# Kernel tuning notes

Measured on AMD Instinct MI355X. Metric: run time of the kernel, lower is better.

## Reference

```python
import jax, jax.numpy as jnp
import numpy as np

B, C, D, E = 2048, 64, 1024, 128
P_INT = 0.0  # p_int=0 -> intervention mask is all zeros (deterministic)


def setup_inputs() -> dict:
    key = jax.random.key(0)
    ks = jax.random.split(key, 16)
    s = lambda k, shape, fan: jax.random.normal(k, shape, jnp.float32) * (1.0 / np.sqrt(fan))
    return {
        "x": jax.random.normal(ks[0], (B, D), jnp.float32),
        "c_int": jax.random.uniform(ks[1], (B, C), jnp.float32),
        # stacked per-concept scorer MLP: Linear(D,D) -> ReLU -> Linear(D,1) -> Sigmoid
        "W1": s(ks[2], (C, D, D), D), "b1": jnp.zeros((C, D), jnp.float32),
        "w2": s(ks[3], (C, D), D), "b2": jnp.zeros((C,), jnp.float32),
        # stacked per-concept embed layer: Linear(D+1, D+1) -> ReLU
        "Wl": s(ks[4], (C, D + 1, D + 1), D + 1), "bl": jnp.zeros((C, D + 1), jnp.float32),
        # shared heads
        "Wmu": s(ks[5], (D + 1, E), D + 1), "bmu": jnp.zeros((E,), jnp.float32),
        "Wlv": s(ks[6], (D + 1, E), D + 1), "blv": jnp.zeros((E,), jnp.float32),
        "proto_pos": jax.random.normal(ks[7], (C, E), jnp.float32),
        "proto_neg": jax.random.normal(ks[8], (C, E), jnp.float32),
    }


def reference(x, c_int, W1, b1, w2, b2, Wl, bl, Wmu, bmu, Wlv, blv, proto_pos, proto_neg):
    # Concept scorers (all concepts batched as one grouped GEMM).
    h = jax.nn.relu(jnp.einsum("bd,cdk->bck", x, W1) + b1)          # [B,C,D]
    c_pred = jax.nn.sigmoid(jnp.einsum("bck,ck->bc", h, w2) + b2)    # [B,C]
    # Per-concept embedding layer on [x ; c_pred].
    xc = jnp.concatenate(
        [jnp.broadcast_to(x[:, None, :], (x.shape[0], C, D)), c_pred[..., None]], axis=-1
    )                                                                # [B,C,D+1]
    emb = jax.nn.relu(jnp.einsum("bck,ckj->bcj", xc, Wl) + bl)       # [B,C,D+1]
    mu = jnp.einsum("bcj,je->bce", emb, Wmu) + bmu                   # [B,C,E]
    logvar = jnp.einsum("bcj,je->bce", emb, Wlv) + blv               # [B,C,E]
    c_emb = mu  # eval mode: no reparameterization noise
    # Intervention blend (mask ~ Bernoulli(p_int); p_int=0 -> zeros, deterministic)
    mask = jnp.zeros_like(c_pred)                                    # [B,C]
    cp = mask * c_int + (1.0 - mask) * c_pred                        # [B,C]
    proto = cp[..., None] * proto_pos + (1.0 - cp[..., None]) * proto_neg  # [B,C,E]
    c_emb = mask[..., None] * proto + (1.0 - mask[..., None]) * c_emb
    return (c_pred, c_emb, mu, logvar)
```

## Files before the change

### kernel.cpp

```cpp
#include <hip/hip_runtime.h>
#include <hip/hip_bf16.h>
#include <cstdint>
#include <cstddef>

#define OFF_CE 131072ull
#define OFF_MU (131072ull + 16777216ull)
#define OFF_LV (131072ull + 33554432ull)

using bf16x8 = __attribute__((ext_vector_type(8))) __bf16;
using s16x8  = __attribute__((ext_vector_type(8))) short;
using f32x4  = __attribute__((ext_vector_type(4))) float;

__device__ __forceinline__ unsigned short f2bf(float x) {
  unsigned u = __builtin_bit_cast(unsigned, x);
  return (unsigned short)((u + 0x7FFFu + ((u >> 16) & 1u)) >> 16);
}
__device__ __forceinline__ float bf2f(unsigned short h) {
  unsigned u = ((unsigned)h) << 16;
  return __builtin_bit_cast(float, u);
}
__device__ __forceinline__ void async16(const void* g, void* l) {
  __builtin_amdgcn_global_load_lds(
      (const __attribute__((address_space(1))) void*)g,
      (__attribute__((address_space(3))) void*)l, 16, 0, 0);
}

struct PX {
  const float *Wl, *Wmu, *Wlv, *b2, *presum, *w2l, *bl1024, *Wlcolf;
  const unsigned short *xb;
  unsigned short *WlT, *WheadT;
  float *whead1024f, *e1024, *pred;
};

template <int ALIGNED, int NT>
__device__ __forceinline__ void tile_tr64(const float* __restrict__ src, int stride,
                                          unsigned short* __restrict__ dst, int t256,
                                          float (*t)[68]) {
#pragma unroll
  for (int i = 0; i < 4; ++i) {
    const int row = (t256 >> 4) + (i << 4);
    const int col4 = (t256 & 15) << 2;
    const float* sp = src + (size_t)row * stride + col4;
    float4 v;
    if constexpr (ALIGNED) {
      v = *(const float4*)sp;
    } else if constexpr (NT) {
      v.x = __builtin_nontemporal_load(sp);
      v.y = __builtin_nontemporal_load(sp + 1);
      v.z = __builtin_nontemporal_load(sp + 2);
      v.w = __builtin_nontemporal_load(sp + 3);
    } else {
      v.x = sp[0]; v.y = sp[1]; v.z = sp[2]; v.w = sp[3];
    }
    *(float4*)&t[row][col4] = v;
  }
  __syncthreads();
  const int n = t256 & 63;
#pragma unroll
  for (int pq = 0; pq < 2; ++pq) {
    const int k8 = ((t256 >> 6) << 3) + (pq << 5);
    unsigned short tmp[8];
#pragma unroll
    for (int j = 0; j < 8; ++j) tmp[j] = f2bf(t[k8 + j][n]);
    *(uint4*)(dst + (size_t)n * 1024 + k8) = *(uint4*)tmp;
  }
}

__global__ __launch_bounds__(256) void prep1_k(const float* __restrict__ W1,
                                               const float* __restrict__ x,
                                               const float* __restrict__ Wl,
                                               const float* __restrict__ bl,
                                               unsigned short* __restrict__ xb,
                                               unsigned short* __restrict__ W1T,
                                               float* __restrict__ wlastf,
                                               float* __restrict__ blpf,
                                               float* __restrict__ Wlcolf,
                                               float* __restrict__ w2l,
                                               float* __restrict__ bl1024) {
  __shared__ float t[64][68];
  const int bid = blockIdx.x;
  const int tid = threadIdx.x;
  if (bid < 16384) {
    const int c = bid >> 8, kt = (bid >> 4) & 15, nt = bid & 15;
    tile_tr64<1, 0>(W1 + ((size_t)c << 20) + ((size_t)(kt << 6) << 10) + (nt << 6), 1024,
                    W1T + ((size_t)c << 20) + ((size_t)(nt << 6) << 10) + (kt << 6), tid, t);
  } else if (bid < 17408) {
    const int idx = (bid - 16384) * 256 + tid;
    const float4* xv = (const float4*)x;
    float4 a = xv[idx * 2], b = xv[idx * 2 + 1];
    unsigned w0 = f2bf(a.x) | ((unsigned)f2bf(a.y) << 16);
    unsigned w1 = f2bf(a.z) | ((unsigned)f2bf(a.w) << 16);
    unsigned w2 = f2bf(b.x) | ((unsigned)f2bf(b.y) << 16);
    unsigned w3 = f2bf(b.z) | ((unsigned)f2bf(b.w) << 16);
    ((uint4*)xb)[idx] = make_uint4(w0, w1, w2, w3);
  } else {
    const int idx = (bid - 17408) * 256 + tid;
    const int c = idx >> 10, j = idx & 1023;
    const float* src = Wl + (size_t)c * 1050625;
    wlastf[idx] = src[(size_t)1024 * 1025 + j];
    blpf[idx]   = bl[(size_t)c * 1025 + j];
    Wlcolf[idx] = src[(size_t)j * 1025 + 1024];
    if (j == 0) {
      w2l[c]    = src[(size_t)1024 * 1025 + 1024];
      bl1024[c] = bl[(size_t)c * 1025 + 1024];
    }
  }
}

__device__ void tail_work(int e, int tid, char* lds, const PX& p) {
  if (e < 512) {
    const int idx = e * 512 + tid;
    const int rr = idx >> 10, k = idx & 1023;
    float v = (rr < 128) ? p.Wmu[(size_t)k * 128 + rr] : p.Wlv[(size_t)k * 128 + (rr - 128)];
    p.WheadT[idx] = f2bf(v);
    if (e == 0 && tid < 256)
      p.whead1024f[tid] = (tid < 128) ? p.Wmu[131072 + tid] : p.Wlv[131072 + (tid - 128)];
    return;
  }
  if (e < 2560) {
    const int b = e - 512;
    const int w = tid >> 6, lane = tid & 63;
    const unsigned short* xr = p.xb + ((size_t)b << 10) + lane * 16;
    s16x8 xv0 = *(const s16x8*)xr;
    s16x8 xv1 = *(const s16x8*)(xr + 8);
    float xf[16];
#pragma unroll
    for (int i = 0; i < 8; ++i) {
      xf[i] = bf2f((unsigned short)xv0[i]);
      xf[8 + i] = bf2f((unsigned short)xv1[i]);
    }
#pragma unroll
    for (int q = 0; q < 8; ++q) {
      const int c = (q << 3) + w;
      const float* wr = p.Wlcolf + (c << 10) + lane * 16;
      float s = 0.f;
#pragma unroll
      for (int q4 = 0; q4 < 4; ++q4) {
        float4 wv = *(const float4*)(wr + q4 * 4);
        s += xf[q4 * 4 + 0] * wv.x + xf[q4 * 4 + 1] * wv.y +
             xf[q4 * 4 + 2] * wv.z + xf[q4 * 4 + 3] * wv.w;
      }
#pragma unroll
      for (int off = 32; off; off >>= 1) s += __shfl_xor(s, off);
      if (lane == 0) ((float*)p.presum)[(c << 11) + b] = s;
    }
    return;
  }
  const int u = e - 2560;
  const int half = tid >> 8, t256 = tid & 255;
  const int tau = (u << 1) + half;
  const int c = tau >> 8, kt = (tau >> 4) & 15, ntl = tau & 15;
  float (*t)[68] = (float(*)[68])(lds + half * (64 * 68 * 4));
  tile_tr64<0, 1>(p.Wl + (size_t)c * 1050625 + (size_t)(kt << 6) * 1025 + (ntl << 6), 1025,
                  p.WlT + ((size_t)c << 20) + ((size_t)(ntl << 6) << 10) + (kt << 6), t256, t);
}


#define BAR() __builtin_amdgcn_s_barrier()
#define LGKM0() do { asm volatile("s_waitcnt lgkmcnt(0)" ::: "memory"); \
                     __builtin_amdgcn_sched_barrier(0); } while (0)
#define VM4() asm volatile("s_waitcnt vmcnt(4)" ::: "memory")
#define VM0() asm volatile("s_waitcnt vmcnt(0)" ::: "memory")

#define STAGEA(h, tt, bidx) do { _Pragma("unroll") for (int q_ = 0; q_ < 2; ++q_) \
  async16(Asrc[q_] + ((size_t)(h) * 128) * K + (size_t)(tt) * 64, \
          &sA[bidx][(h) * 8192 + chnk[q_]]); } while (0)
#define STAGEB(h, tt, bidx) do { _Pragma("unroll") for (int q_ = 0; q_ < 2; ++q_) \
  async16(Bsrc[q_] + ((size_t)(h) * 128) * K + (size_t)(tt) * 64, \
          &sB[bidx][(h) * 8192 + chnk[q_]]); } while (0)

#define LOADA(mh, bidx) do { _Pragma("unroll") for (int i_ = 0; i_ < 4; ++i_) { \
  const int ro_ = ((mh) * 128 + wm64 + i_ * 16 + l15) << 6; \
  a[i_][0] = *(const bf16x8*)&sA[bidx][ro_ + ccx0]; \
  a[i_][1] = *(const bf16x8*)&sA[bidx][ro_ + ccx1]; } } while (0)

#define LOADB(nh, bb, bidx) do { _Pragma("unroll") for (int j_ = 0; j_ < 2; ++j_) { \
  const int ro_ = ((nh) * 128 + wn32 + j_ * 16 + l15) << 6; \
  bb[j_][0] = *(const bf16x8*)&sB[bidx][ro_ + ccx0]; \
  bb[j_][1] = *(const bf16x8*)&sB[bidx][ro_ + ccx1]; } } while (0)

#define MMAQ(mh, nh, bb) do { _Pragma("unroll") for (int i_ = 0; i_ < 4; ++i_) \
  _Pragma("unroll") for (int j_ = 0; j_ < 2; ++j_) { \
    acc[(mh)*4+i_][(nh)*2+j_] = __builtin_amdgcn_mfma_f32_16x16x32_bf16( \
        a[i_][0], bb[j_][0], acc[(mh)*4+i_][(nh)*2+j_], 0, 0, 0); \
    acc[(mh)*4+i_][(nh)*2+j_] = __builtin_amdgcn_mfma_f32_16x16x32_bf16( \
        a[i_][1], bb[j_][1], acc[(mh)*4+i_][(nh)*2+j_], 0, 0, 0); \
  } } while (0)

#define KSTEP(t_, cb_, nb_) do { \
    LOADA(0, cb_); LOADB(0, b0, cb_); STAGEA(0, (t_) + 1, nb_); \
    BAR(); LGKM0(); \
    __builtin_amdgcn_s_setprio(1); MMAQ(0, 0, b0); __builtin_amdgcn_s_setprio(0); \
    VM4(); BAR(); \
    LOADB(1, b1, cb_); STAGEB(0, (t_) + 1, nb_); \
    BAR(); LGKM0(); \
    __builtin_amdgcn_s_setprio(1); MMAQ(0, 1, b1); __builtin_amdgcn_s_setprio(0); \
    VM4(); BAR(); \
    LOADA(1, cb_); STAGEB(1, (t_) + 1, nb_); \
    BAR(); LGKM0(); \
    __builtin_amdgcn_s_setprio(1); MMAQ(1, 1, b1); __builtin_amdgcn_s_setprio(0); \
    BAR(); \
    STAGEA(1, (t_) + 1, nb_); \
    BAR(); \
    __builtin_amdgcn_s_setprio(1); MMAQ(1, 0, b0); __builtin_amdgcn_s_setprio(0); \
    VM4(); BAR(); \
  } while (0)

template <int MODE, int K>
__global__ __launch_bounds__(512, 2) void gemm8p_k(
    const unsigned short* __restrict__ A, const unsigned short* __restrict__ BT,
    const float* __restrict__ e0, const float* __restrict__ e1,
    const float* __restrict__ e2, const float* __restrict__ e3,
    unsigned short* __restrict__ obf, float* __restrict__ ofl, PX p) {
  __shared__ unsigned short sA[2][16384];
  __shared__ unsigned short sB[2][16384];

  constexpr int GX = (MODE == 2) ? 1 : 4;
  constexpr int GY = (MODE == 2) ? 512 : 8;
  constexpr int NWG = GX * GY * ((MODE == 2) ? 1 : 64);

  const int tid = threadIdx.x;

  int rbid;
  if constexpr (MODE == 0) {
    const int bidR = blockIdx.x;
    if (bidR >= 2048) { tail_work(bidR - 2048, tid, (char*)&sA[0][0], p); return; }
    rbid = bidR;
  } else {
    rbid = blockIdx.x + GX * (blockIdx.y + GY * blockIdx.z);
  }

  const int lane = tid & 63;
  const int wid = tid >> 6;
  const int wm = wid >> 2, wn = wid & 3;
  const int l15 = lane & 15, l4 = lane >> 4;
  const int wm64 = wm << 6, wn32 = wn << 5;

  const int bid = (rbid & 7) * (NWG >> 3) + (rbid >> 3);
  const int bx = bid % GX;
  const int by = (bid / GX) % GY;
  const int c = bid / (GX * GY);

  const int n0 = bx << 8;
  const int m0 = by << 8;

  const unsigned short* Ab = A;
  const unsigned short* Bb;
  if constexpr (MODE == 2) Bb = BT;
  else                     Bb = BT + ((size_t)c << 20);

  int rloc[2], csrc[2], chnk[2];
  const unsigned short* Asrc[2];
  const unsigned short* Bsrc[2];
#pragma unroll
  for (int q = 0; q < 2; ++q) {
    const int s = ((wid << 1) + q) * 64 + lane;
    rloc[q] = s >> 3;
    csrc[q] = ((s & 7) ^ ((s >> 3) & 7)) << 3;
    chnk[q] = ((wid << 1) + q) << 9;
    Asrc[q] = Ab + (size_t)(m0 + rloc[q]) * K + csrc[q];
    Bsrc[q] = Bb + (size_t)(n0 + rloc[q]) * K + csrc[q];
  }

  const int xorv = l15 & 7;
  const int ccx0 = (l4 ^ xorv) << 3;
  const int ccx1 = ((4 + l4) ^ xorv) << 3;

  f32x4 acc[8][4];
#pragma unroll
  for (int i = 0; i < 8; ++i)
#pragma unroll
    for (int j = 0; j < 4; ++j) acc[i][j] = (f32x4)(0.f);

  bf16x8 a[4][2], b0[2][2], b1[2][2];

  static_assert(K == 1024, "schedule assumes 16 K-tiles");

  STAGEA(0, 0, 0); STAGEB(0, 0, 0); STAGEB(1, 0, 0); STAGEA(1, 0, 0);
  VM0();
  BAR();

#pragma unroll 1
  for (int tt = 0; tt < 7; ++tt) {
    const int t0 = tt << 1;
    KSTEP(t0, 0, 1);
    KSTEP(t0 + 1, 1, 0);
  }
  KSTEP(14, 0, 1);

  {
    VM0();
    BAR();
    LOADA(0, 1);
    LOADB(0, b0, 1);
    LGKM0();
    __builtin_amdgcn_s_setprio(1);
    MMAQ(0, 0, b0);
    __builtin_amdgcn_s_setprio(0);
    LOADB(1, b1, 1);
    LGKM0();
    __builtin_amdgcn_s_setprio(1);
    MMAQ(0, 1, b1);
    __builtin_amdgcn_s_setprio(0);
    LOADA(1, 1);
    LGKM0();
    __builtin_amdgcn_s_setprio(1);
    MMAQ(1, 1, b1);
    MMAQ(1, 0, b0);
    __builtin_amdgcn_s_setprio(0);
  }

  int coln[2][2];
#pragma unroll
  for (int nh = 0; nh < 2; ++nh)
#pragma unroll
    for (int j = 0; j < 2; ++j) coln[nh][j] = n0 + nh * 128 + wn32 + j * 16 + l15;

  if constexpr (MODE == 0) {
    float bias[2][2], w2v[2][2];
#pragma unroll
    for (int nh = 0; nh < 2; ++nh)
#pragma unroll
      for (int j = 0; j < 2; ++j) {
        bias[nh][j] = e0[(c << 10) + coln[nh][j]];
        w2v[nh][j]  = e1[(c << 10) + coln[nh][j]];
      }
    float* partL = (float*)&sA[0][0];
#pragma unroll
    for (int mh = 0; mh < 2; ++mh)
#pragma unroll
      for (int i = 0; i < 4; ++i)
#pragma unroll
        for (int rr = 0; rr < 4; ++rr) {
          float s = 0.f;
#pragma unroll
          for (int nh = 0; nh < 2; ++nh)
#pragma unroll
            for (int j = 0; j < 2; ++j) {
              float v = fmaxf(acc[mh * 4 + i][nh * 2 + j][rr] + bias[nh][j], 0.f);
              s += v * w2v[nh][j];
            }
          s += __shfl_xor(s, 1); s += __shfl_xor(s, 2);
          s += __shfl_xor(s, 4); s += __shfl_xor(s, 8);
          if (l15 == 0) partL[wid * 128 + mh * 64 + i * 16 + (l4 << 2) + rr] = s;
        }
    __syncthreads();
    if (tid < 256) {
      const int r = tid;
      const int mh_ = r >> 7, wmr = (r >> 6) & 1, low = r & 63;
      float s2 = 0.f;
#pragma unroll
      for (int wn2 = 0; wn2 < 4; ++wn2) s2 += partL[(wmr * 4 + wn2) * 128 + mh_ * 64 + low];
      ofl[(((size_t)(bx << 6) + c) << 11) + m0 + r] = s2;
    }
  } else if constexpr (MODE == 1) {
    float* cpL = (float*)&sA[0][0];
    if (tid < 256) {
      const int b = m0 + tid;
      float s = p.b2[c];
#pragma unroll
      for (int q = 0; q < 4; ++q) s += e2[(((size_t)(q << 6) + c) << 11) + b];
      float pv = 1.f / (1.f + expf(-s));
      cpL[tid] = pv;
      if (bx == 0) {
        p.pred[((size_t)b << 6) + c] = pv;
        p.e1024[(c << 11) + b] =
            fmaxf(p.presum[(c << 11) + b] + pv * p.w2l[c] + p.bl1024[c], 0.f);
      }
    }
    __syncthreads();
    float wl4[2][2], bb4[2][2];
#pragma unroll
    for (int nh = 0; nh < 2; ++nh)
#pragma unroll
      for (int j = 0; j < 2; ++j) {
        wl4[nh][j] = e0[(c << 10) + coln[nh][j]];
        bb4[nh][j] = e1[(c << 10) + coln[nh][j]];
      }
#pragma unroll
    for (int mh = 0; mh < 2; ++mh)
#pragma unroll
      for (int i = 0; i < 4; ++i)
#pragma unroll
        for (int rr = 0; rr < 4; ++rr) {
          const int rl = mh * 128 + wm64 + i * 16 + (l4 << 2) + rr;
          const int row = m0 + rl;
          const float cp = cpL[rl];
          unsigned short* orow = obf + (((size_t)(c << 11) + row) << 10);
#pragma unroll
          for (int nh = 0; nh < 2; ++nh)
#pragma unroll
            for (int j = 0; j < 2; ++j) {
              float v = acc[mh * 4 + i][nh * 2 + j][rr] + cp * wl4[nh][j] + bb4[nh][j];
              orow[coln[nh][j]] = f2bf(fmaxf(v, 0.f));
            }
        }
  } else {
    float bias[2][2], wh[2][2];
#pragma unroll
    for (int nh = 0; nh < 2; ++nh)
#pragma unroll
      for (int j = 0; j < 2; ++j) {
        bias[nh][j] = (nh == 0) ? e0[coln[0][j]] : e1[coln[1][j] - 128];
        wh[nh][j]   = e3[coln[nh][j]];
      }
#pragma unroll
    for (int mh = 0; mh < 2; ++mh)
#pragma unroll
      for (int i = 0; i < 4; ++i)
#pragma unroll
        for (int rr = 0; rr < 4; ++rr) {
          const int rid = m0 + mh * 128 + wm64 + i * 16 + (l4 << 2) + rr;
          const int cc = rid >> 11, b = rid & 2047;
          const float ev = e2[rid];
          const size_t ib = (((size_t)b << 6) + cc) << 7;
#pragma unroll
          for (int j = 0; j < 2; ++j) {
            float v = acc[mh * 4 + i][j][rr] + bias[0][j] + ev * wh[0][j];
            ofl[OFF_MU + ib + coln[0][j]] = v;
            ofl[OFF_CE + ib + coln[0][j]] = v;
          }
#pragma unroll
          for (int j = 0; j < 2; ++j) {
            float v = acc[mh * 4 + i][2 + j][rr] + bias[1][j] + ev * wh[1][j];
            ofl[OFF_LV + ib + (coln[1][j] - 128)] = v;
          }
        }
  }
}


extern "C" void kernel_launch(void* const* d_in, const int* in_sizes, int n_in,
                              void* d_out, int out_size, void* d_ws, size_t ws_size,
                              hipStream_t stream) {
  const float* x   = (const float*)d_in[0];
  const float* W1  = (const float*)d_in[2];
  const float* b1  = (const float*)d_in[3];
  const float* w2  = (const float*)d_in[4];
  const float* b2  = (const float*)d_in[5];
  const float* Wl  = (const float*)d_in[6];
  const float* bl  = (const float*)d_in[7];
  const float* Wmu = (const float*)d_in[8];
  const float* bmu = (const float*)d_in[9];
  const float* Wlv = (const float*)d_in[10];
  const float* blv = (const float*)d_in[11];
  float* out = (float*)d_out;

  char* ws = (char*)d_ws;
  size_t off = 0;
  auto take = [&](size_t bytes) { char* r = ws + off; off += bytes; return r; };
  unsigned short* xb     = (unsigned short*)take(4194304);
  unsigned short* W1T    = (unsigned short*)take(134217728);
  unsigned short* WlT    = (unsigned short*)take(134217728);
  float* wlastf          = (float*)take(262144);
  float* blpf            = (float*)take(262144);
  float* Wlcolf          = (float*)take(262144);
  float* w2l             = (float*)take(512);
  float* bl1024          = (float*)take(512);
  unsigned short* WheadT = (unsigned short*)take(524288);
  float* whead1024f      = (float*)take(1024);
  float* presum          = (float*)take(524288);
  float* spart           = (float*)take(2097152);
  float* e1024f          = (float*)take(524288);
  unsigned short* emb    = (unsigned short*)take(268435456);

  PX p;
  p.Wl = Wl; p.Wmu = Wmu; p.Wlv = Wlv; p.b2 = b2;
  p.presum = presum; p.w2l = w2l; p.bl1024 = bl1024; p.Wlcolf = Wlcolf;
  p.xb = xb; p.WlT = WlT; p.WheadT = WheadT;
  p.whead1024f = whead1024f; p.e1024 = e1024f; p.pred = out;

  prep1_k<<<17664, 256, 0, stream>>>(W1, x, Wl, bl, xb, W1T, wlastf, blpf, Wlcolf, w2l, bl1024);
  gemm8p_k<0, 1024><<<12800, 512, 0, stream>>>(xb, W1T, b1, w2, nullptr, nullptr,
                                               nullptr, spart, p);
  gemm8p_k<1, 1024><<<dim3(4, 8, 64), 512, 0, stream>>>(xb, WlT, wlastf, blpf, spart, nullptr,
                                                        emb, nullptr, p);
  gemm8p_k<2, 1024><<<dim3(1, 512, 1), 512, 0, stream>>>(emb, WheadT, bmu, blv, e1024f,
                                                         whead1024f, nullptr, out, p);
}
```

Measured before the change: 952.1 us.

## Batch Wl transpose tiles per block and use nontemporal loads in prep

The Wl transpose tail work now handles four 64x64 tiles per 512-thread block, two per half, with all global loads issued before any LDS staging, so the grid tail shrinks. The transpose tiles run first in the tail order and the Wlcol presum work is moved to the end. Prep loads of W1, x and the Wl row and column now use nontemporal vector loads to keep streamed weights from polluting cache. The trade-off is higher register and LDS use per block, plus different scheduling overlap between the tail work and the main GEMM.

```diff
diff --git a/kernel.cpp b/kernel.cpp
--- a/kernel.cpp
+++ b/kernel.cpp
@@ -23,6 +23,9 @@
   __builtin_amdgcn_global_load_lds(
       (const __attribute__((address_space(1))) void*)g,
       (__attribute__((address_space(3))) void*)l, 16, 0, 0);
+}
+__device__ __forceinline__ f32x4 nt_load4(const float* p4) {
+  return __builtin_nontemporal_load((const f32x4*)p4);
 }
 
 struct PX {
@@ -41,9 +44,11 @@
     const int row = (t256 >> 4) + (i << 4);
     const int col4 = (t256 & 15) << 2;
     const float* sp = src + (size_t)row * stride + col4;
-    float4 v;
-    if constexpr (ALIGNED) {
-      v = *(const float4*)sp;
+    f32x4 v;
+    if constexpr (ALIGNED && NT) {
+      v = nt_load4(sp);
+    } else if constexpr (ALIGNED) {
+      v = *(const f32x4*)sp;
     } else if constexpr (NT) {
       v.x = __builtin_nontemporal_load(sp);
       v.y = __builtin_nontemporal_load(sp + 1);
@@ -52,7 +57,7 @@
     } else {
       v.x = sp[0]; v.y = sp[1]; v.z = sp[2]; v.w = sp[3];
     }
-    *(float4*)&t[row][col4] = v;
+    *(f32x4*)&t[row][col4] = v;
   }
   __syncthreads();
   const int n = t256 & 63;
@@ -82,12 +87,12 @@
   const int tid = threadIdx.x;
   if (bid < 16384) {
     const int c = bid >> 8, kt = (bid >> 4) & 15, nt = bid & 15;
-    tile_tr64<1, 0>(W1 + ((size_t)c << 20) + ((size_t)(kt << 6) << 10) + (nt << 6), 1024,
+    tile_tr64<1, 1>(W1 + ((size_t)c << 20) + ((size_t)(kt << 6) << 10) + (nt << 6), 1024,
                     W1T + ((size_t)c << 20) + ((size_t)(nt << 6) << 10) + (kt << 6), tid, t);
   } else if (bid < 17408) {
     const int idx = (bid - 16384) * 256 + tid;
-    const float4* xv = (const float4*)x;
-    float4 a = xv[idx * 2], b = xv[idx * 2 + 1];
+    f32x4 a = nt_load4(x + (size_t)idx * 8);
+    f32x4 b = nt_load4(x + (size_t)idx * 8 + 4);
     unsigned w0 = f2bf(a.x) | ((unsigned)f2bf(a.y) << 16);
     unsigned w1 = f2bf(a.z) | ((unsigned)f2bf(a.w) << 16);
     unsigned w2 = f2bf(b.x) | ((unsigned)f2bf(b.y) << 16);
@@ -97,9 +102,9 @@
     const int idx = (bid - 17408) * 256 + tid;
     const int c = idx >> 10, j = idx & 1023;
     const float* src = Wl + (size_t)c * 1050625;
-    wlastf[idx] = src[(size_t)1024 * 1025 + j];
+    wlastf[idx] = __builtin_nontemporal_load(&src[(size_t)1024 * 1025 + j]);
     blpf[idx]   = bl[(size_t)c * 1025 + j];
-    Wlcolf[idx] = src[(size_t)j * 1025 + 1024];
+    Wlcolf[idx] = __builtin_nontemporal_load(&src[(size_t)j * 1025 + 1024]);
     if (j == 0) {
       w2l[c]    = src[(size_t)1024 * 1025 + 1024];
       bl1024[c] = bl[(size_t)c * 1025 + 1024];
@@ -108,51 +113,98 @@
 }
 
 __device__ void tail_work(int e, int tid, char* lds, const PX& p) {
-  if (e < 512) {
-    const int idx = e * 512 + tid;
+  if (e < 4096) {
+    const int g = tid >> 8, t256 = tid & 255;
+    const int tau0 = (e << 2) + (g << 1);
+    float (*tA)[68] = (float(*)[68])(lds + g * 34816);
+    float (*tB)[68] = (float(*)[68])(lds + g * 34816 + 17408);
+    const int c0 = tau0 >> 8, kt0 = (tau0 >> 4) & 15, nt0 = tau0 & 15;
+    const int tau1 = tau0 + 1;
+    const int c1 = tau1 >> 8, kt1 = (tau1 >> 4) & 15, nt1 = tau1 & 15;
+    const float* srcA = p.Wl + (size_t)c0 * 1050625 + (size_t)(kt0 << 6) * 1025 + (nt0 << 6);
+    const float* srcB = p.Wl + (size_t)c1 * 1050625 + (size_t)(kt1 << 6) * 1025 + (nt1 << 6);
+    unsigned short* dstA = p.WlT + ((size_t)c0 << 20) + ((size_t)(nt0 << 6) << 10) + (kt0 << 6);
+    unsigned short* dstB = p.WlT + ((size_t)c1 << 20) + ((size_t)(nt1 << 6) << 10) + (kt1 << 6);
+    const int row = t256 >> 4;
+    const int col4 = (t256 & 15) << 2;
+    f32x4 vA[4], vB[4];
+#pragma unroll
+    for (int i = 0; i < 4; ++i) {
+      const float* q = srcA + (size_t)(row + (i << 4)) * 1025 + col4;
+      vA[i].x = __builtin_nontemporal_load(q);
+      vA[i].y = __builtin_nontemporal_load(q + 1);
+      vA[i].z = __builtin_nontemporal_load(q + 2);
+      vA[i].w = __builtin_nontemporal_load(q + 3);
+    }
+#pragma unroll
+    for (int i = 0; i < 4; ++i) {
+      const float* q = srcB + (size_t)(row + (i << 4)) * 1025 + col4;
+      vB[i].x = __builtin_nontemporal_load(q);
+      vB[i].y = __builtin_nontemporal_load(q + 1);
+      vB[i].z = __builtin_nontemporal_load(q + 2);
+      vB[i].w = __builtin_nontemporal_load(q + 3);
+    }
+#pragma unroll
+    for (int i = 0; i < 4; ++i) *(f32x4*)&tA[row + (i << 4)][col4] = vA[i];
+    __syncthreads();
+#pragma unroll
+    for (int i = 0; i < 4; ++i) *(f32x4*)&tB[row + (i << 4)][col4] = vB[i];
+    const int n = t256 & 63;
+#pragma unroll
+    for (int pq = 0; pq < 2; ++pq) {
+      const int k8 = ((t256 >> 6) << 3) + (pq << 5);
+      unsigned short tmp[8];
+#pragma unroll
+      for (int j = 0; j < 8; ++j) tmp[j] = f2bf(tA[k8 + j][n]);
+      *(uint4*)(dstA + (size_t)n * 1024 + k8) = *(uint4*)tmp;
+    }
+    __syncthreads();
+#pragma unroll
+    for (int pq = 0; pq < 2; ++pq) {
+      const int k8 = ((t256 >> 6) << 3) + (pq << 5);
+      unsigned short tmp[8];
+#pragma unroll
+      for (int j = 0; j < 8; ++j) tmp[j] = f2bf(tB[k8 + j][n]);
+      *(uint4*)(dstB + (size_t)n * 1024 + k8) = *(uint4*)tmp;
+    }
+    return;
+  }
+  if (e < 4608) {
+    const int we = e - 4096;
+    const int idx = we * 512 + tid;
     const int rr = idx >> 10, k = idx & 1023;
     float v = (rr < 128) ? p.Wmu[(size_t)k * 128 + rr] : p.Wlv[(size_t)k * 128 + (rr - 128)];
     p.WheadT[idx] = f2bf(v);
-    if (e == 0 && tid < 256)
+    if (we == 0 && tid < 256)
       p.whead1024f[tid] = (tid < 128) ? p.Wmu[131072 + tid] : p.Wlv[131072 + (tid - 128)];
     return;
   }
-  if (e < 2560) {
-    const int b = e - 512;
-    const int w = tid >> 6, lane = tid & 63;
-    const unsigned short* xr = p.xb + ((size_t)b << 10) + lane * 16;
-    s16x8 xv0 = *(const s16x8*)xr;
-    s16x8 xv1 = *(const s16x8*)(xr + 8);
-    float xf[16];
-#pragma unroll
-    for (int i = 0; i < 8; ++i) {
-      xf[i] = bf2f((unsigned short)xv0[i]);
-      xf[8 + i] = bf2f((unsigned short)xv1[i]);
-    }
-#pragma unroll
-    for (int q = 0; q < 8; ++q) {
-      const int c = (q << 3) + w;
-      const float* wr = p.Wlcolf + (c << 10) + lane * 16;
-      float s = 0.f;
-#pragma unroll
-      for (int q4 = 0; q4 < 4; ++q4) {
-        float4 wv = *(const float4*)(wr + q4 * 4);
-        s += xf[q4 * 4 + 0] * wv.x + xf[q4 * 4 + 1] * wv.y +
-             xf[q4 * 4 + 2] * wv.z + xf[q4 * 4 + 3] * wv.w;
-      }
-#pragma unroll
-      for (int off = 32; off; off >>= 1) s += __shfl_xor(s, off);
-      if (lane == 0) ((float*)p.presum)[(c << 11) + b] = s;
-    }
-    return;
-  }
-  const int u = e - 2560;
-  const int half = tid >> 8, t256 = tid & 255;
-  const int tau = (u << 1) + half;
-  const int c = tau >> 8, kt = (tau >> 4) & 15, ntl = tau & 15;
-  float (*t)[68] = (float(*)[68])(lds + half * (64 * 68 * 4));
-  tile_tr64<0, 1>(p.Wl + (size_t)c * 1050625 + (size_t)(kt << 6) * 1025 + (ntl << 6), 1025,
-                  p.WlT + ((size_t)c << 20) + ((size_t)(ntl << 6) << 10) + (kt << 6), t256, t);
+  const int b = e - 4608;
+  const int w = tid >> 6, lane = tid & 63;
+  const unsigned short* xr = p.xb + ((size_t)b << 10) + lane * 16;
+  s16x8 xv0 = *(const s16x8*)xr;
+  s16x8 xv1 = *(const s16x8*)(xr + 8);
+  float xf[16];
+#pragma unroll
+  for (int i = 0; i < 8; ++i) {
+    xf[i] = bf2f((unsigned short)xv0[i]);
+    xf[8 + i] = bf2f((unsigned short)xv1[i]);
+  }
+#pragma unroll
+  for (int q = 0; q < 8; ++q) {
+    const int c = (q << 3) + w;
+    const float* wr = p.Wlcolf + (c << 10) + lane * 16;
+    float s = 0.f;
+#pragma unroll
+    for (int q4 = 0; q4 < 4; ++q4) {
+      f32x4 wv = *(const f32x4*)(wr + q4 * 4);
+      s += xf[q4 * 4 + 0] * wv.x + xf[q4 * 4 + 1] * wv.y +
+           xf[q4 * 4 + 2] * wv.z + xf[q4 * 4 + 3] * wv.w;
+    }
+#pragma unroll
+    for (int off = 32; off; off >>= 1) s += __shfl_xor(s, off);
+    if (lane == 0) ((float*)p.presum)[(c << 11) + b] = s;
+  }
 }
 
 
@@ -471,8 +523,8 @@
   p.whead1024f = whead1024f; p.e1024 = e1024f; p.pred = out;
 
   prep1_k<<<17664, 256, 0, stream>>>(W1, x, Wl, bl, xb, W1T, wlastf, blpf, Wlcolf, w2l, bl1024);
-  gemm8p_k<0, 1024><<<12800, 512, 0, stream>>>(xb, W1T, b1, w2, nullptr, nullptr,
-                                               nullptr, spart, p);
+  gemm8p_k<0, 1024><<<8704, 512, 0, stream>>>(xb, W1T, b1, w2, nullptr, nullptr,
+                                              nullptr, spart, p);
   gemm8p_k<1, 1024><<<dim3(4, 8, 64), 512, 0, stream>>>(xb, WlT, wlastf, blpf, spart, nullptr,
                                                         emb, nullptr, p);
   gemm8p_k<2, 1024><<<dim3(1, 512, 1), 512, 0, stream>>>(emb, WheadT, bmu, blv, e1024f,
```

Measured after the change: 932.3 us. -2.1%, faster.
